# Performance work log

Hardware: AMD Instinct MI355X
Metric: run time of the kernel (lower is better)

The kernel has to match this reference:

```python
import jax, jax.numpy as jnp
import numpy as np

N, E = 8192, 262144
IN_DIM, OUT_DIM = 256, 256


def setup_inputs() -> dict:
    key = jax.random.key(0)
    k = jax.random.split(key, 7)
    x = jax.random.normal(k[0], (N, IN_DIM), dtype=jnp.float32)
    edge_index = jax.random.randint(k[1], (2, E), 0, N, dtype=jnp.int64)
    # parameters (nn.Linear stores weight as (out, in); bias=False everywhere)
    W = jax.random.normal(k[2], (OUT_DIM, IN_DIM), dtype=jnp.float32) / np.sqrt(IN_DIM)
    a_src = jax.random.normal(k[3], (OUT_DIM,), dtype=jnp.float32) / np.sqrt(OUT_DIM)
    a_dst = jax.random.normal(k[4], (OUT_DIM,), dtype=jnp.float32) / np.sqrt(OUT_DIM)
    gamma = jnp.ones((OUT_DIM,), dtype=jnp.float32)
    beta = jnp.zeros((OUT_DIM,), dtype=jnp.float32)
    return {"x": x, "edge_index": edge_index, "W": W, "a_src": a_src,
            "a_dst": a_dst, "gamma": gamma, "beta": beta}


def reference(x, edge_index, W, a_src, a_dst, gamma, beta):
    h = x @ W.T                                     # (N, D)
    src, dst = edge_index[0], edge_index[1]
    s_src = h @ a_src                               # (N,) attn_src logits
    s_dst = h @ a_dst                               # (N,)
    e = jax.nn.leaky_relu(s_src[src] + s_dst[dst], negative_slope=0.2)  # (E,)
    n = x.shape[0]
    # dense scatter: attn[dst, src] = e (duplicate edges overwrite, like torch)
    attn = jnp.zeros((n, n), dtype=x.dtype).at[dst, src].set(e)
    attn = jax.nn.softmax(attn + (attn == 0).astype(x.dtype) * -1e9, axis=-1)
    attn = attn * (attn > 1e-6).astype(x.dtype)
    out = attn @ h                                  # (N, D)
    z = jax.nn.elu(out) + h
    # LayerNorm (eps=1e-5, biased variance, matching torch)
    mean = jnp.mean(z, axis=-1, keepdims=True)
    var = jnp.var(z, axis=-1, keepdims=True)
    return gamma * (z - mean) * jax.lax.rsqrt(var + 1e-5) + beta
```

## Files before the change

### kernel.cpp

```cpp
#include <hip/hip_runtime.h>
#include <math.h>

#define N_NODES 8192
#define EDGES   262144
#define D       256
#define ROWCAP  128
#define PITCH   68


__global__ __launch_bounds__(256)
void gemm_h(const float* __restrict__ x, const float* __restrict__ W,
            const float* __restrict__ a_src, const float* __restrict__ a_dst,
            float* __restrict__ h, float* __restrict__ s_src,
            float* __restrict__ s_dst) {
  __shared__ float As[32][PITCH];
  __shared__ float Bs[32][PITCH];
  const int bm = blockIdx.x * 64;
  const int bj = blockIdx.y * 64;
  const int tid = threadIdx.x;
  const int tr = tid >> 4, tc = tid & 15;
  float acc[4][4] = {{0.f}};
  for (int k0 = 0; k0 < D; k0 += 32) {
#pragma unroll
    for (int f = 0; f < 2; ++f) {
      int idx = tid + f * 256;
      int r = idx >> 3, c4 = (idx & 7) << 2;
      float4 va = *reinterpret_cast<const float4*>(&x[(size_t)(bm + r) * D + k0 + c4]);
      As[c4][r] = va.x; As[c4 + 1][r] = va.y; As[c4 + 2][r] = va.z; As[c4 + 3][r] = va.w;
      float4 vb = *reinterpret_cast<const float4*>(&W[(size_t)(bj + r) * D + k0 + c4]);
      Bs[c4][r] = vb.x; Bs[c4 + 1][r] = vb.y; Bs[c4 + 2][r] = vb.z; Bs[c4 + 3][r] = vb.w;
    }
    __syncthreads();
#pragma unroll
    for (int k = 0; k < 32; ++k) {
      float4 a4 = *reinterpret_cast<const float4*>(&As[k][tr * 4]);
      float4 b4 = *reinterpret_cast<const float4*>(&Bs[k][tc * 4]);
      float a[4] = {a4.x, a4.y, a4.z, a4.w};
      float b[4] = {b4.x, b4.y, b4.z, b4.w};
#pragma unroll
      for (int i = 0; i < 4; ++i)
#pragma unroll
        for (int j = 0; j < 4; ++j)
          acc[i][j] = fmaf(a[i], b[j], acc[i][j]);
    }
    __syncthreads();
  }
  float4 asv = *reinterpret_cast<const float4*>(&a_src[bj + tc * 4]);
  float4 adv = *reinterpret_cast<const float4*>(&a_dst[bj + tc * 4]);
#pragma unroll
  for (int i = 0; i < 4; ++i) {
    float4 v = make_float4(acc[i][0], acc[i][1], acc[i][2], acc[i][3]);
    *reinterpret_cast<float4*>(&h[(size_t)(bm + tr * 4 + i) * D + bj + tc * 4]) = v;
    float ps = v.x * asv.x + v.y * asv.y + v.z * asv.z + v.w * asv.w;
    float pd = v.x * adv.x + v.y * adv.y + v.z * adv.z + v.w * adv.w;
#pragma unroll
    for (int off = 8; off; off >>= 1) {
      ps += __shfl_down(ps, off, 16);
      pd += __shfl_down(pd, off, 16);
    }
    if (tc == 0) {
      atomicAdd(&s_src[bm + tr * 4 + i], ps);
      atomicAdd(&s_dst[bm + tr * 4 + i], pd);
    }
  }
}

__global__ __launch_bounds__(256)
void scatter_kernel(const int* __restrict__ ei, int* __restrict__ fill,
                    int* __restrict__ csr) {
  int lane = threadIdx.x & 63;
  unsigned long long b = __ballot(ei[lane * 2 + 1] == 0);
  int is64 = (b == 0xFFFFFFFFFFFFFFFFull) ? 1 : 0;
  int e = blockIdx.x * 256 + threadIdx.x;
  int src, dst;
  if (is64) { src = ei[2 * e];  dst = ei[2 * (EDGES + e)]; }
  else      { src = ei[e];      dst = ei[EDGES + e]; }
  int p = atomicAdd(&fill[dst], 1);
  if (p < ROWCAP) csr[dst * ROWCAP + p] = src;
}

__global__ __launch_bounds__(256)
void row_fused(const float* __restrict__ h, const float* __restrict__ s_src,
               const float* __restrict__ s_dst, const int* __restrict__ fill,
               const int* __restrict__ csr, const float* __restrict__ gamma,
               const float* __restrict__ beta, float* __restrict__ out) {
  __shared__ int   s_idx[4][ROWCAP];
  __shared__ float s_w[4][ROWCAP];
  const int w    = threadIdx.x >> 6;
  const int lane = threadIdx.x & 63;
  const int row  = blockIdx.x * 4 + w;
  int len = fill[row];
  if (len > ROWCAP) len = ROWCAP;
  const int len_pad = (len + 3) & ~3;
  const float sd = s_dst[row];

  for (int i = lane; i < len; i += 64) s_idx[w][i] = csr[row * ROWCAP + i];
  __syncthreads();

  float lmax = -3.0e38f;
  for (int i = lane; i < len; i += 64) {
    int s = s_idx[w][i];
    bool dup = false;
    for (int j = 0; j < i; ++j)
      if (s_idx[w][j] == s) { dup = true; break; }
    float v;
    if (dup) {
      v = -3.0e38f;
    } else {
      v = s_src[s] + sd;
      v = (v >= 0.f) ? v : 0.2f * v;
      if (v == 0.0f) v = -3.0e38f;
    }
    s_w[w][i] = v;
    lmax = fmaxf(lmax, v);
  }
#pragma unroll
  for (int off = 32; off; off >>= 1) lmax = fmaxf(lmax, __shfl_xor(lmax, off, 64));

  float lsum = 0.f;
  for (int i = lane; i < len; i += 64) {
    float e = expf(s_w[w][i] - lmax);
    s_w[w][i] = e;
    lsum += e;
  }
#pragma unroll
  for (int off = 32; off; off >>= 1) lsum += __shfl_xor(lsum, off, 64);
  float inv = (lsum > 0.f) ? (1.0f / lsum) : 0.f;
  for (int i = lane; i < len; i += 64) {
    float ww = s_w[w][i] * inv;
    s_w[w][i] = (ww > 1e-6f) ? ww : 0.f;
  }
  for (int i = len + lane; i < len_pad; i += 64) { s_w[w][i] = 0.f; s_idx[w][i] = 0; }
  __syncthreads();

  float4 acc = make_float4(0.f, 0.f, 0.f, 0.f);
  for (int i = 0; i < len_pad; i += 4) {
    float w0 = s_w[w][i], w1 = s_w[w][i + 1], w2 = s_w[w][i + 2], w3 = s_w[w][i + 3];
    const float4 h0 = *reinterpret_cast<const float4*>(&h[(size_t)s_idx[w][i]     * D + lane * 4]);
    const float4 h1 = *reinterpret_cast<const float4*>(&h[(size_t)s_idx[w][i + 1] * D + lane * 4]);
    const float4 h2 = *reinterpret_cast<const float4*>(&h[(size_t)s_idx[w][i + 2] * D + lane * 4]);
    const float4 h3 = *reinterpret_cast<const float4*>(&h[(size_t)s_idx[w][i + 3] * D + lane * 4]);
    acc.x = fmaf(w0, h0.x, fmaf(w1, h1.x, fmaf(w2, h2.x, fmaf(w3, h3.x, acc.x))));
    acc.y = fmaf(w0, h0.y, fmaf(w1, h1.y, fmaf(w2, h2.y, fmaf(w3, h3.y, acc.y))));
    acc.z = fmaf(w0, h0.z, fmaf(w1, h1.z, fmaf(w2, h2.z, fmaf(w3, h3.z, acc.z))));
    acc.w = fmaf(w0, h0.w, fmaf(w1, h1.w, fmaf(w2, h2.w, fmaf(w3, h3.w, acc.w))));
  }

  const float4 hr = *reinterpret_cast<const float4*>(&h[(size_t)row * D + lane * 4]);
  float4 z;
  z.x = ((acc.x > 0.f) ? acc.x : expm1f(acc.x)) + hr.x;
  z.y = ((acc.y > 0.f) ? acc.y : expm1f(acc.y)) + hr.y;
  z.z = ((acc.z > 0.f) ? acc.z : expm1f(acc.z)) + hr.z;
  z.w = ((acc.w > 0.f) ? acc.w : expm1f(acc.w)) + hr.w;

  float s1 = z.x + z.y + z.z + z.w;
#pragma unroll
  for (int off = 32; off; off >>= 1) s1 += __shfl_xor(s1, off, 64);
  float mean = s1 * (1.0f / 256.0f);
  float dx = z.x - mean, dy = z.y - mean, dz = z.z - mean, dw = z.w - mean;
  float s2 = dx * dx + dy * dy + dz * dz + dw * dw;
#pragma unroll
  for (int off = 32; off; off >>= 1) s2 += __shfl_xor(s2, off, 64);
  float rs = rsqrtf(s2 * (1.0f / 256.0f) + 1e-5f);

  const float4 gm = *reinterpret_cast<const float4*>(&gamma[lane * 4]);
  const float4 bt = *reinterpret_cast<const float4*>(&beta[lane * 4]);
  float4 o;
  o.x = gm.x * dx * rs + bt.x;
  o.y = gm.y * dy * rs + bt.y;
  o.z = gm.z * dz * rs + bt.z;
  o.w = gm.w * dw * rs + bt.w;
  *reinterpret_cast<float4*>(&out[(size_t)row * D + lane * 4]) = o;
}

extern "C" void kernel_launch(void* const* d_in, const int* in_sizes, int n_in,
                              void* d_out, int out_size, void* d_ws, size_t ws_size,
                              hipStream_t stream) {
  const float* x     = (const float*)d_in[0];
  const int*   ei    = (const int*)d_in[1];
  const float* W     = (const float*)d_in[2];
  const float* a_src = (const float*)d_in[3];
  const float* a_dst = (const float*)d_in[4];
  const float* gamma = (const float*)d_in[5];
  const float* beta  = (const float*)d_in[6];
  float* out = (float*)d_out;

  char* ws = (char*)d_ws;
  int*   fill   = (int*)(ws);
  float* s_src  = (float*)(ws + 32768);
  float* s_dst  = (float*)(ws + 65536);
  int*   csr    = (int*)(ws + 98304);
  float* h      = (float*)(ws + 4292608);
  if (ws_size < 12681216) return;

  hipMemsetAsync(ws, 0, 98304, stream);
  gemm_h<<<dim3(N_NODES / 64, D / 64), 256, 0, stream>>>(x, W, a_src, a_dst,
                                                         h, s_src, s_dst);
  scatter_kernel<<<EDGES / 256, 256, 0, stream>>>(ei, fill, csr);
  row_fused<<<N_NODES / 4, 256, 0, stream>>>(h, s_src, s_dst, fill, csr, gamma, beta, out);
}
```

Measured before the change: 137.9 us.

## Use split-bf16 MFMA GEMM for projection and unroll gather by eight

Replaces the FP32 SIMT tiled GEMM with a matrix-core GEMM. A pre-pass splits x and W into bf16 hi/lo pairs, and the kernel runs three bf16 MFMAs per tile to keep close to fp32 accuracy. The goal is to move the 8192x256x256 projection onto matrix cores, at the cost of an extra split kernel, extra workspace traffic and no LDS reuse, since operands are loaded straight from global memory. The aggregation loop is also unrolled to eight neighbors per step so more gather loads are in flight.

```diff
diff --git a/kernel.cpp b/kernel.cpp
--- a/kernel.cpp
+++ b/kernel.cpp
@@ -5,62 +5,90 @@
 #define EDGES   262144
 #define D       256
 #define ROWCAP  128
-#define PITCH   68
-
-
-__global__ __launch_bounds__(256)
-void gemm_h(const float* __restrict__ x, const float* __restrict__ W,
-            const float* __restrict__ a_src, const float* __restrict__ a_dst,
-            float* __restrict__ h, float* __restrict__ s_src,
-            float* __restrict__ s_dst) {
-  __shared__ float As[32][PITCH];
-  __shared__ float Bs[32][PITCH];
-  const int bm = blockIdx.x * 64;
+
+typedef __attribute__((ext_vector_type(8))) short bf8;
+typedef __attribute__((ext_vector_type(4))) float f32x4;
+
+
+__device__ __forceinline__ ushort f2bf(float f) {
+  unsigned u = __float_as_uint(f);
+  return (ushort)((u + 0x7FFF + ((u >> 16) & 1)) >> 16);
+}
+__device__ __forceinline__ float bf2f(ushort s) {
+  return __uint_as_float((unsigned)s << 16);
+}
+
+#define XQ 524288
+#define WQ 16384
+__global__ __launch_bounds__(256)
+void split_kernel(const float* __restrict__ x, const float* __restrict__ W,
+                  ushort* __restrict__ xhi, ushort* __restrict__ xlo,
+                  ushort* __restrict__ whi, ushort* __restrict__ wlo) {
+  int i = blockIdx.x * 256 + threadIdx.x;
+  const float4* src; ushort *dh, *dl; int j;
+  if (i < XQ) { src = (const float4*)x; dh = xhi; dl = xlo; j = i; }
+  else        { src = (const float4*)W; dh = whi; dl = wlo; j = i - XQ; }
+  float4 v = src[j];
+  ushort4 h4, l4;
+  h4.x = f2bf(v.x); l4.x = f2bf(v.x - bf2f(h4.x));
+  h4.y = f2bf(v.y); l4.y = f2bf(v.y - bf2f(h4.y));
+  h4.z = f2bf(v.z); l4.z = f2bf(v.z - bf2f(h4.z));
+  h4.w = f2bf(v.w); l4.w = f2bf(v.w - bf2f(h4.w));
+  *reinterpret_cast<ushort4*>(dh + (size_t)j * 4) = h4;
+  *reinterpret_cast<ushort4*>(dl + (size_t)j * 4) = l4;
+}
+
+__global__ __launch_bounds__(256)
+void gemm_mfma(const ushort* __restrict__ xhi, const ushort* __restrict__ xlo,
+               const ushort* __restrict__ whi, const ushort* __restrict__ wlo,
+               const float* __restrict__ a_src, const float* __restrict__ a_dst,
+               float* __restrict__ h, float* __restrict__ s_src,
+               float* __restrict__ s_dst) {
+  const int wv = threadIdx.x >> 6, lane = threadIdx.x & 63;
+  const int bm = blockIdx.x * 64 + wv * 16;
   const int bj = blockIdx.y * 64;
-  const int tid = threadIdx.x;
-  const int tr = tid >> 4, tc = tid & 15;
-  float acc[4][4] = {{0.f}};
+  const int r = lane & 15, kg = lane >> 4;
+  const f32x4 z4 = {0.f, 0.f, 0.f, 0.f};
+  f32x4 acc[4] = {z4, z4, z4, z4};
+  const size_t arow = (size_t)(bm + r) * D;
   for (int k0 = 0; k0 < D; k0 += 32) {
-#pragma unroll
-    for (int f = 0; f < 2; ++f) {
-      int idx = tid + f * 256;
-      int r = idx >> 3, c4 = (idx & 7) << 2;
-      float4 va = *reinterpret_cast<const float4*>(&x[(size_t)(bm + r) * D + k0 + c4]);
-      As[c4][r] = va.x; As[c4 + 1][r] = va.y; As[c4 + 2][r] = va.z; As[c4 + 3][r] = va.w;
-      float4 vb = *reinterpret_cast<const float4*>(&W[(size_t)(bj + r) * D + k0 + c4]);
-      Bs[c4][r] = vb.x; Bs[c4 + 1][r] = vb.y; Bs[c4 + 2][r] = vb.z; Bs[c4 + 3][r] = vb.w;
-    }
-    __syncthreads();
-#pragma unroll
-    for (int k = 0; k < 32; ++k) {
-      float4 a4 = *reinterpret_cast<const float4*>(&As[k][tr * 4]);
-      float4 b4 = *reinterpret_cast<const float4*>(&Bs[k][tc * 4]);
-      float a[4] = {a4.x, a4.y, a4.z, a4.w};
-      float b[4] = {b4.x, b4.y, b4.z, b4.w};
-#pragma unroll
-      for (int i = 0; i < 4; ++i)
-#pragma unroll
-        for (int j = 0; j < 4; ++j)
-          acc[i][j] = fmaf(a[i], b[j], acc[i][j]);
-    }
-    __syncthreads();
-  }
-  float4 asv = *reinterpret_cast<const float4*>(&a_src[bj + tc * 4]);
-  float4 adv = *reinterpret_cast<const float4*>(&a_dst[bj + tc * 4]);
-#pragma unroll
-  for (int i = 0; i < 4; ++i) {
-    float4 v = make_float4(acc[i][0], acc[i][1], acc[i][2], acc[i][3]);
-    *reinterpret_cast<float4*>(&h[(size_t)(bm + tr * 4 + i) * D + bj + tc * 4]) = v;
-    float ps = v.x * asv.x + v.y * asv.y + v.z * asv.z + v.w * asv.w;
-    float pd = v.x * adv.x + v.y * adv.y + v.z * adv.z + v.w * adv.w;
-#pragma unroll
-    for (int off = 8; off; off >>= 1) {
-      ps += __shfl_down(ps, off, 16);
-      pd += __shfl_down(pd, off, 16);
-    }
-    if (tc == 0) {
-      atomicAdd(&s_src[bm + tr * 4 + i], ps);
-      atomicAdd(&s_dst[bm + tr * 4 + i], pd);
+    const int ko = k0 + kg * 8;
+    bf8 ahi = *reinterpret_cast<const bf8*>(xhi + arow + ko);
+    bf8 alo = *reinterpret_cast<const bf8*>(xlo + arow + ko);
+#pragma unroll
+    for (int ct = 0; ct < 4; ++ct) {
+      const size_t boff = (size_t)(bj + ct * 16 + r) * D + ko;
+      bf8 bhi = *reinterpret_cast<const bf8*>(whi + boff);
+      bf8 blo = *reinterpret_cast<const bf8*>(wlo + boff);
+      acc[ct] = __builtin_amdgcn_mfma_f32_16x16x32_bf16(ahi, bhi, acc[ct], 0, 0, 0);
+      acc[ct] = __builtin_amdgcn_mfma_f32_16x16x32_bf16(ahi, blo, acc[ct], 0, 0, 0);
+      acc[ct] = __builtin_amdgcn_mfma_f32_16x16x32_bf16(alo, bhi, acc[ct], 0, 0, 0);
+    }
+  }
+  float pS[4] = {0.f, 0.f, 0.f, 0.f}, pD[4] = {0.f, 0.f, 0.f, 0.f};
+#pragma unroll
+  for (int ct = 0; ct < 4; ++ct) {
+    const int col = bj + ct * 16 + r;
+    const float av = a_src[col], dv = a_dst[col];
+#pragma unroll
+    for (int reg = 0; reg < 4; ++reg) {
+      const float c = acc[ct][reg];
+      h[(size_t)(bm + kg * 4 + reg) * D + col] = c;
+      pS[reg] = fmaf(c, av, pS[reg]);
+      pD[reg] = fmaf(c, dv, pD[reg]);
+    }
+  }
+#pragma unroll
+  for (int reg = 0; reg < 4; ++reg) {
+    float ps = pS[reg], pd = pD[reg];
+#pragma unroll
+    for (int off = 1; off < 16; off <<= 1) {
+      ps += __shfl_xor(ps, off, 64);
+      pd += __shfl_xor(pd, off, 64);
+    }
+    if (r == 0) {
+      atomicAdd(&s_src[bm + kg * 4 + reg], ps);
+      atomicAdd(&s_dst[bm + kg * 4 + reg], pd);
     }
   }
 }
@@ -91,7 +119,7 @@
   const int row  = blockIdx.x * 4 + w;
   int len = fill[row];
   if (len > ROWCAP) len = ROWCAP;
-  const int len_pad = (len + 3) & ~3;
+  const int len_pad = (len + 7) & ~7;
   const float sd = s_dst[row];
 
   for (int i = lane; i < len; i += 64) s_idx[w][i] = csr[row * ROWCAP + i];
@@ -134,16 +162,20 @@
   __syncthreads();
 
   float4 acc = make_float4(0.f, 0.f, 0.f, 0.f);
-  for (int i = 0; i < len_pad; i += 4) {
-    float w0 = s_w[w][i], w1 = s_w[w][i + 1], w2 = s_w[w][i + 2], w3 = s_w[w][i + 3];
-    const float4 h0 = *reinterpret_cast<const float4*>(&h[(size_t)s_idx[w][i]     * D + lane * 4]);
-    const float4 h1 = *reinterpret_cast<const float4*>(&h[(size_t)s_idx[w][i + 1] * D + lane * 4]);
-    const float4 h2 = *reinterpret_cast<const float4*>(&h[(size_t)s_idx[w][i + 2] * D + lane * 4]);
-    const float4 h3 = *reinterpret_cast<const float4*>(&h[(size_t)s_idx[w][i + 3] * D + lane * 4]);
-    acc.x = fmaf(w0, h0.x, fmaf(w1, h1.x, fmaf(w2, h2.x, fmaf(w3, h3.x, acc.x))));
-    acc.y = fmaf(w0, h0.y, fmaf(w1, h1.y, fmaf(w2, h2.y, fmaf(w3, h3.y, acc.y))));
-    acc.z = fmaf(w0, h0.z, fmaf(w1, h1.z, fmaf(w2, h2.z, fmaf(w3, h3.z, acc.z))));
-    acc.w = fmaf(w0, h0.w, fmaf(w1, h1.w, fmaf(w2, h2.w, fmaf(w3, h3.w, acc.w))));
+  for (int i = 0; i < len_pad; i += 8) {
+    float wg[8]; float4 hv[8];
+#pragma unroll
+    for (int u = 0; u < 8; ++u) {
+      wg[u] = s_w[w][i + u];
+      hv[u] = *reinterpret_cast<const float4*>(&h[(size_t)s_idx[w][i + u] * D + lane * 4]);
+    }
+#pragma unroll
+    for (int u = 0; u < 8; ++u) {
+      acc.x = fmaf(wg[u], hv[u].x, acc.x);
+      acc.y = fmaf(wg[u], hv[u].y, acc.y);
+      acc.z = fmaf(wg[u], hv[u].z, acc.z);
+      acc.w = fmaf(wg[u], hv[u].w, acc.w);
+    }
   }
 
   const float4 hr = *reinterpret_cast<const float4*>(&h[(size_t)row * D + lane * 4]);
@@ -186,16 +218,21 @@
   float* out = (float*)d_out;
 
   char* ws = (char*)d_ws;
-  int*   fill   = (int*)(ws);
-  float* s_src  = (float*)(ws + 32768);
-  float* s_dst  = (float*)(ws + 65536);
-  int*   csr    = (int*)(ws + 98304);
-  float* h      = (float*)(ws + 4292608);
-  if (ws_size < 12681216) return;
+  int*    fill  = (int*)(ws);
+  float*  s_src = (float*)(ws + 32768);
+  float*  s_dst = (float*)(ws + 65536);
+  int*    csr   = (int*)(ws + 98304);
+  float*  h     = (float*)(ws + 4292608);
+  ushort* xhi   = (ushort*)(ws + 12681216);
+  ushort* xlo   = (ushort*)(ws + 16875520);
+  ushort* whi   = (ushort*)(ws + 21069824);
+  ushort* wlo   = (ushort*)(ws + 21200896);
+  if (ws_size < 21331968) return;
 
   hipMemsetAsync(ws, 0, 98304, stream);
-  gemm_h<<<dim3(N_NODES / 64, D / 64), 256, 0, stream>>>(x, W, a_src, a_dst,
-                                                         h, s_src, s_dst);
+  split_kernel<<<(XQ + WQ) / 256, 256, 0, stream>>>(x, W, xhi, xlo, whi, wlo);
   scatter_kernel<<<EDGES / 256, 256, 0, stream>>>(ei, fill, csr);
+  gemm_mfma<<<dim3(N_NODES / 64, D / 64), 256, 0, stream>>>(xhi, xlo, whi, wlo,
+                                                            a_src, a_dst, h, s_src, s_dst);
   row_fused<<<N_NODES / 4, 256, 0, stream>>>(h, s_src, s_dst, fill, csr, gamma, beta, out);
 }
```

Result: no change. 139.8 us (+1.3%).
